# Optimization experiments

Hardware: AMD Instinct MI355X
Metric: run time of the kernel (lower is better)

Reference implementation:

```python
import jax, jax.numpy as jnp
import numpy as np

EPS = 1e-5  # GroupNorm eps


def setup_inputs() -> dict:
    key = jax.random.key(0)
    ks = jax.random.split(key, 12)
    D, H, I = 512, 8, 64
    B, L = 2, 1024
    g = 0.01  # xavier gain used in reset_parameters
    inp = {
        "x": jax.random.normal(ks[0], (B, L, D), jnp.float32),
        "w_z": jax.random.normal(ks[1], (D, D), jnp.float32) * g,
        "b_z": jnp.zeros((D,), jnp.float32),
        "w_za": jax.random.normal(ks[2], (D, D), jnp.float32) * g,
        "b_za": jnp.zeros((D,), jnp.float32),
        "w_ang": jax.random.normal(ks[3], (D, H), jnp.float32) * g,
        "b_ang": jnp.zeros((H,), jnp.float32),
        "w_abs": jax.random.normal(ks[4], (D, H), jnp.float32) * g,
        "b_abs": jnp.zeros((H,), jnp.float32),
        "w_y": jax.random.normal(ks[5], (D, D), jnp.float32) * g,
        "b_y": jnp.zeros((D,), jnp.float32),
        "w_ya": jax.random.normal(ks[6], (D, D), jnp.float32) * g,
        "b_ya": jnp.zeros((D,), jnp.float32),
        "gn_w": jnp.ones((H,), jnp.float32),
        "gn_b": jnp.zeros((H,), jnp.float32),
        "lc_r": jax.random.normal(ks[7], (H, I), jnp.float32),
        "lc_i": jax.random.normal(ks[8], (H, I), jnp.float32),
    }
    return inp


def reference(x, w_z, b_z, w_za, b_za, w_ang, b_ang, w_abs, b_abs,
              w_y, b_y, w_ya, b_ya, gn_w, gn_b, lc_r, lc_i):
    B, L, D = x.shape
    H = gn_w.shape[0]
    I = D // H
    silu = jax.nn.silu
    xf = x.astype(jnp.float32)

    # gated value, promoted to complex:  [B, L, H, I]
    z = ((xf @ w_z + b_z) * silu(xf @ w_za + b_za)).astype(jnp.complex64).reshape(B, L, H, I)

    # per-head log-decay phazor: [B, L, H] complex
    scale = (0.001 ** jnp.linspace(0.0, 1.0, H)).astype(jnp.float32)
    ln_ph = (silu(xf @ w_ang + b_ang) * 1j - jax.nn.sigmoid(xf @ w_abs + b_abs)) * scale

    # FFT of ones => circular conv with ones = cumulative sum along axis 1
    ones_fft = jnp.fft.fft(jnp.ones((L,), jnp.float32), n=2 * L)

    # ln_phazor repeated over m then tril(-1) over the LAST TWO dims (m, h),
    # exactly matching torch.Tensor.tril semantics on a 'b l m h' tensor.
    masked = jnp.tril(jnp.broadcast_to(ln_ph[:, :, None, :], (B, L, L, H)), -1)
    mfft = jnp.fft.fft(masked, n=2 * L, axis=1)
    mconv = jnp.fft.ifft(mfft * ones_fft[None, :, None, None], axis=1)[:, :L]
    ph_masked = jnp.tril(jnp.exp(mconv))  # tril over (m, h)

    h_inner = jnp.einsum('blmh,bmhi->blhi', ph_masked, z)

    pfft = jnp.fft.fft(ln_ph, n=2 * L, axis=1)
    pconv = jnp.fft.ifft(pfft * ones_fft[None, :, None], axis=1)[:, :L]
    last_conv = lc_r + 1j * lc_i  # [H, I] complex (last_conv_init broadcast over batch)
    h_cross = jnp.exp(pconv)[..., None] * last_conv[None, None]  # [B, L, H, I]

    h = (h_inner + h_cross).real  # [B, L, H, I]

    # GroupNorm(H groups, H channels) on (B*L, H, I): per-(sample, head) norm over I
    mean = h.mean(axis=-1, keepdims=True)
    var = h.var(axis=-1, keepdims=True)
    hn = (h - mean) / jnp.sqrt(var + EPS) * gn_w[:, None] + gn_b[:, None]
    h_norm = hn.reshape(B, L, D)

    y = (h_norm @ w_y + b_y) * silu(xf @ w_ya + b_ya)
    return y.astype(x.dtype)
```

## Files before the change

kernel.cpp:

```cpp
#include <hip/hip_runtime.h>
#include <math.h>

#define D_ 512
#define H_ 8
#define I_ 64
#define L_ 1024

typedef __attribute__((ext_vector_type(8))) short short8;
typedef __attribute__((ext_vector_type(4))) float f32x4;

__device__ __forceinline__ float sigmoidf_(float x) { return 1.f / (1.f + expf(-x)); }
__device__ __forceinline__ float siluf_(float x) { return x / (1.f + expf(-x)); }

__device__ __forceinline__ unsigned short f2bf(float f) {
    unsigned u = __float_as_uint(f);
    u += 0x7fffu + ((u >> 16) & 1u);
    return (unsigned short)(u >> 16);
}
__device__ __forceinline__ float bf2f(unsigned short v) {
    return __uint_as_float((unsigned)v << 16);
}

__global__ __launch_bounds__(256) void k1_prep(
    const float* __restrict__ x,
    const float* __restrict__ w0, const float* __restrict__ w1,
    const float* __restrict__ w2, const float* __restrict__ w3,
    unsigned short* __restrict__ t0, unsigned short* __restrict__ t1,
    unsigned short* __restrict__ t2, unsigned short* __restrict__ t3,
    const float* __restrict__ w_ang, const float* __restrict__ b_ang,
    const float* __restrict__ w_abs, const float* __restrict__ b_abs,
    float* __restrict__ a_out, float* __restrict__ r_out)
{
    __shared__ float sm[64][65];
    const int tid = threadIdx.x;
    const int bid = blockIdx.x;
    if (bid < 256) {
        int zsel = bid >> 6, tile = bid & 63;
        const float* src = zsel == 0 ? w0 : zsel == 1 ? w1 : zsel == 2 ? w2 : w3;
        unsigned short* dst = zsel == 0 ? t0 : zsel == 1 ? t1 : zsel == 2 ? t2 : t3;
        const int k0 = (tile >> 3) * 64, n0 = (tile & 7) * 64;
#pragma unroll
        for (int i = 0; i < 16; ++i) {
            int idx = tid + i * 256;
            int rr = idx >> 6, cc = idx & 63;
            sm[rr][cc] = src[(size_t)(k0 + rr) * 512 + n0 + cc];
        }
        __syncthreads();
#pragma unroll
        for (int i = 0; i < 16; ++i) {
            int idx = tid + i * 256;
            int rr = idx >> 6, cc = idx & 63;
            dst[(size_t)(n0 + rr) * 512 + k0 + cc] = f2bf(sm[cc][rr]);
        }
        return;
    }
    {
        int t = bid - 256;
        const int s = tid & 3, c = (tid >> 2) & 15, r = tid >> 6;
        const int n = t * 4 + r;
        const int h = c & 7;
        const float* wp = (c < 8) ? w_ang : w_abs;
        const float* xr = x + (size_t)n * D_;
        float acc = 0.f;
#pragma unroll 4
        for (int i = 0; i < 128; ++i) {
            int k = i * 4 + s;
            acc = fmaf(xr[k], wp[k * H_ + h], acc);
        }
        acc += __shfl_xor(acc, 1);
        acc += __shfl_xor(acc, 2);
        if (s == 0) {
            const float scale = expf(-6.9077552789821368f * (h * (1.0f / 7.0f)));
            if (c < 8) { float p = acc + b_ang[h]; a_out[(size_t)n * H_ + h] = siluf_(p) * scale; }
            else       { float p = acc + b_abs[h]; r_out[(size_t)n * H_ + h] = sigmoidf_(p) * scale; }
        }
    }
}

__global__ __launch_bounds__(256) void k2_gemm3_scan(
    const float* __restrict__ x,
    const unsigned short* __restrict__ Wz, const unsigned short* __restrict__ Wza,
    const unsigned short* __restrict__ Wya,
    const float* __restrict__ b_z, const float* __restrict__ b_za, const float* __restrict__ b_ya,
    unsigned short* __restrict__ gateb, float* __restrict__ Zs_part, float* __restrict__ zdiag,
    const float* __restrict__ a_arr, const float* __restrict__ r_arr,
    float* __restrict__ Si, float* __restrict__ Sr)
{
    __shared__ short As[2][2048];
    __shared__ short Bs[2][3][2048];
    __shared__ float red[64][8];
    __shared__ float2 buf[2][256];
    const int tid = threadIdx.x;

    if ((int)blockIdx.y < 2) {
        const int b = blockIdx.y, h = blockIdx.x;
        float2 v[4];
        float2 run = make_float2(0.f, 0.f);
        const size_t base = ((size_t)b * L_ + tid * 4) * H_ + h;
#pragma unroll
        for (int j = 0; j < 4; ++j) {
            run.x += a_arr[base + j * H_];
            run.y += r_arr[base + j * H_];
            v[j] = run;
        }
        buf[0][tid] = run;
        __syncthreads();
        int src = 0;
        for (int off = 1; off < 256; off <<= 1) {
            float2 val = buf[src][tid];
            if (tid >= off) { float2 p = buf[src][tid - off]; val.x += p.x; val.y += p.y; }
            buf[src ^ 1][tid] = val;
            src ^= 1;
            __syncthreads();
        }
        float2 excl = make_float2(0.f, 0.f);
        if (tid > 0) excl = buf[src][tid - 1];
#pragma unroll
        for (int j = 0; j < 4; ++j) {
            Si[base + j * H_] = v[j].x + excl.x;
            Sr[base + j * H_] = -(v[j].y + excl.y);
        }
        return;
    }

    const int lane = tid & 63, w = tid >> 6;
    const int wm = w >> 1, wn = w & 1;
    const int bx = blockIdx.x;
    const int rblk = (int)blockIdx.y - 2;
    const int row0 = rblk * 64, col0 = bx * 64;

    const f32x4 zf = {0.f, 0.f, 0.f, 0.f};
    f32x4 accz[2][2], accza[2][2], accya[2][2];
#pragma unroll
    for (int a = 0; a < 2; ++a)
#pragma unroll
        for (int bq = 0; bq < 2; ++bq) { accz[a][bq] = zf; accza[a][bq] = zf; accya[a][bq] = zf; }

    const int sr = tid >> 2, sc = tid & 3;
    const int sld = sr * 64 + ((sc ^ ((sr >> 1) & 3)) << 4);
    const float* gAx = x + (size_t)(row0 + sr) * 512 + sc * 8;
    const unsigned short* gWz  = Wz  + (size_t)(col0 + sr) * 512 + sc * 8;
    const unsigned short* gWza = Wza + (size_t)(col0 + sr) * 512 + sc * 8;
    const unsigned short* gWya = Wya + (size_t)(col0 + sr) * 512 + sc * 8;

    float4 ra0, ra1; int4 rz, rza, rya;
#define K2_LOAD(K) { ra0 = *(const float4*)(gAx + (K)); ra1 = *(const float4*)(gAx + (K) + 4); \
                     rz  = *(const int4*)(gWz  + (K)); rza = *(const int4*)(gWza + (K)); \
                     rya = *(const int4*)(gWya + (K)); }
#define K2_WRITE(BUF) { short8 ab; \
                        ab[0]=(short)f2bf(ra0.x); ab[1]=(short)f2bf(ra0.y); \
                        ab[2]=(short)f2bf(ra0.z); ab[3]=(short)f2bf(ra0.w); \
                        ab[4]=(short)f2bf(ra1.x); ab[5]=(short)f2bf(ra1.y); \
                        ab[6]=(short)f2bf(ra1.z); ab[7]=(short)f2bf(ra1.w); \
                        *(short8*)((char*)As[BUF] + sld) = ab; \
                        *(int4*)((char*)Bs[BUF][0] + sld) = rz; \
                        *(int4*)((char*)Bs[BUF][1] + sld) = rza; \
                        *(int4*)((char*)Bs[BUF][2] + sld) = rya; }

    K2_LOAD(0);
    K2_WRITE(0);
    K2_LOAD(32);
    __syncthreads();

    int cur = 0;
    for (int s = 0; s < 16; ++s) {
        if (s < 15) {
            K2_WRITE(cur ^ 1);
            if (s < 14) K2_LOAD((s + 2) * 32);
        }
        short8 af[2], bz[2], bza[2], bya[2];
#pragma unroll
        for (int fi = 0; fi < 2; ++fi) {
            int rr = wm * 32 + fi * 16 + (lane & 15);
            int off = rr * 64 + ((((lane >> 4)) ^ ((rr >> 1) & 3)) << 4);
            af[fi] = *(const short8*)((const char*)As[cur] + off);
        }
#pragma unroll
        for (int fj = 0; fj < 2; ++fj) {
            int rr = wn * 32 + fj * 16 + (lane & 15);
            int off = rr * 64 + ((((lane >> 4)) ^ ((rr >> 1) & 3)) << 4);
            bz[fj]  = *(const short8*)((const char*)Bs[cur][0] + off);
            bza[fj] = *(const short8*)((const char*)Bs[cur][1] + off);
            bya[fj] = *(const short8*)((const char*)Bs[cur][2] + off);
        }
#pragma unroll
        for (int fi = 0; fi < 2; ++fi)
#pragma unroll
            for (int fj = 0; fj < 2; ++fj) {
                accz[fi][fj]  = __builtin_amdgcn_mfma_f32_16x16x32_bf16(af[fi], bz[fj],  accz[fi][fj],  0, 0, 0);
                accza[fi][fj] = __builtin_amdgcn_mfma_f32_16x16x32_bf16(af[fi], bza[fj], accza[fi][fj], 0, 0, 0);
                accya[fi][fj] = __builtin_amdgcn_mfma_f32_16x16x32_bf16(af[fi], bya[fj], accya[fi][fj], 0, 0, 0);
            }
        __syncthreads();
        cur ^= 1;
    }

    const bool first = (rblk & 15) == 0;
    const int b8 = (rblk >> 4) * 8;
#pragma unroll
    for (int fj = 0; fj < 2; ++fj) {
        float lsum = 0.f;
        int lc = wn * 32 + fj * 16 + (lane & 15);
        int col = col0 + lc;
        float Bz = b_z[col], Bza = b_za[col], Bya = b_ya[col];
#pragma unroll
        for (int fi = 0; fi < 2; ++fi) {
#pragma unroll
            for (int q = 0; q < 4; ++q) {
                int lr = wm * 32 + fi * 16 + ((lane >> 4) << 2) + q;
                int row = row0 + lr;
                float pz = accz[fi][fj][q] + Bz;
                float pza = accza[fi][fj][q] + Bza;
                float v = pz * siluf_(pza);
                gateb[(size_t)row * 512 + col] = f2bf(siluf_(accya[fi][fj][q] + Bya));
                if (!first || lr > bx) lsum += v;
                if (first && lr == bx) zdiag[(b8 + bx) * 64 + lc] = v;
            }
        }
        red[lc][wm * 4 + (lane >> 4)] = lsum;
    }
    __syncthreads();
    if (tid < 64) {
        float s = 0.f;
#pragma unroll
        for (int j = 0; j < 8; ++j) s += red[tid][j];
        Zs_part[((size_t)rblk * 8 + bx) * 64 + tid] = s;
    }
}

__global__ __launch_bounds__(512) void k3_hgn_gemm_y(
    const unsigned short* __restrict__ Wy, const float* __restrict__ b_y,
    const unsigned short* __restrict__ gateb,
    const float* __restrict__ Sr, const float* __restrict__ Si,
    const float* __restrict__ Zs_part, const float* __restrict__ zdiag,
    const float* __restrict__ lc_r, const float* __restrict__ lc_i,
    const float* __restrict__ gn_w, const float* __restrict__ gn_b,
    float* __restrict__ y)
{
    __shared__ unsigned short hA[64][520];
    __shared__ short Bs[2][2048];
    __shared__ float Cr[8][65], Ci[8][65], Zd[8][65];
    const int tid = threadIdx.x;
    const int lane = tid & 63, w = tid >> 6;
    const int row0 = blockIdx.y * 64, col0 = blockIdx.x * 64;
    const int b = row0 >> 10;

    const int brow = tid >> 3, bsc = tid & 7;
    const size_t gB = (size_t)(col0 + brow) * 512 + bsc * 4;
    const int bwr = brow * 64 + (((bsc >> 1) ^ ((brow >> 1) & 3)) << 4) + (bsc & 1) * 8;
    int2 rw0 = *(const int2*)(Wy + gB);
    int2 rw1 = *(const int2*)(Wy + gB + 32);

    {
        int h = tid >> 6, i = tid & 63;
        float s = 0.f;
#pragma unroll
        for (int rb = 0; rb < 16; ++rb)
            s += Zs_part[(((size_t)b * 16 + rb) * 8 + h) * 64 + i];
        Cr[h][i] = s + lc_r[h * 64 + i];
        Ci[h][i] = lc_i[h * 64 + i];
        Zd[h][i] = zdiag[((size_t)b * 8 + h) * 64 + i];
    }
    __syncthreads();

    {
        const int r = tid >> 3, h = tid & 7;
        const int row = row0 + r;
        const float sr = Sr[(size_t)row * 8 + h];
        const float si = Si[(size_t)row * 8 + h];
        const float er = expf(sr);
        const float ca = er * cosf(si), sb = er * sinf(si);
        float sum = 0.f, sq = 0.f;
#pragma unroll 8
        for (int i = 0; i < 64; ++i) {
            float hv = Zd[h][i] + ca * Cr[h][i] - sb * Ci[h][i];
            sum += hv; sq += hv * hv;
        }
        const float mean = sum * (1.f / 64.f);
        const float inv = rsqrtf(sq * (1.f / 64.f) - mean * mean + 1e-5f);
        const float gw = gn_w[h] * inv;
        const float gb = gn_b[h] - mean * gw;
#pragma unroll
        for (int s8 = 0; s8 < 8; ++s8) {
            short8 pk;
#pragma unroll
            for (int j = 0; j < 8; ++j) {
                int i = s8 * 8 + j;
                float hv = Zd[h][i] + ca * Cr[h][i] - sb * Ci[h][i];
                pk[j] = (short)f2bf(hv * gw + gb);
            }
            int slot = (s8 + h) & 7;
            *(short8*)((char*)&hA[r][0] + h * 128 + slot * 16) = pk;
        }
    }
    *(int2*)((char*)Bs[0] + bwr) = rw0;
    __syncthreads();

    const int wm = w >> 2, wn = w & 3;
    const f32x4 zf = {0.f, 0.f, 0.f, 0.f};
    f32x4 acc[2] = {zf, zf};

    int cur = 0;
    for (int s = 0; s < 16; ++s) {
        if (s < 15) {
            *(int2*)((char*)Bs[cur ^ 1] + bwr) = rw1;
            if (s < 14) rw1 = *(const int2*)(Wy + gB + (s + 2) * 32);
        }
        const int k0 = s * 32;
        short8 af[2], bf;
        const int hk = k0 >> 6;
        const int t = ((k0 & 32) >> 3) + (lane >> 4);
        const int slot = (t + hk) & 7;
#pragma unroll
        for (int fi = 0; fi < 2; ++fi) {
            int rr = wm * 32 + fi * 16 + (lane & 15);
            af[fi] = *(const short8*)((const char*)&hA[rr][0] + hk * 128 + slot * 16);
        }
        {
            int rr = wn * 16 + (lane & 15);
            bf = *(const short8*)((const char*)Bs[cur] + rr * 64 + (((lane >> 4) ^ ((rr >> 1) & 3)) << 4));
        }
        acc[0] = __builtin_amdgcn_mfma_f32_16x16x32_bf16(af[0], bf, acc[0], 0, 0, 0);
        acc[1] = __builtin_amdgcn_mfma_f32_16x16x32_bf16(af[1], bf, acc[1], 0, 0, 0);
        __syncthreads();
        cur ^= 1;
    }

    const int col = col0 + wn * 16 + (lane & 15);
    const float By = b_y[col];
#pragma unroll
    for (int fi = 0; fi < 2; ++fi)
#pragma unroll
        for (int q = 0; q < 4; ++q) {
            int row = row0 + wm * 32 + fi * 16 + ((lane >> 4) << 2) + q;
            size_t idx = (size_t)row * 512 + col;
            y[idx] = (acc[fi][q] + By) * bf2f(gateb[idx]);
        }
}

extern "C" void kernel_launch(void* const* d_in, const int* in_sizes, int n_in,
                              void* d_out, int out_size, void* d_ws, size_t ws_size,
                              hipStream_t stream) {
    (void)n_in; (void)out_size; (void)ws_size;
    const float* x     = (const float*)d_in[0];
    const float* w_z   = (const float*)d_in[1];
    const float* b_z   = (const float*)d_in[2];
    const float* w_za  = (const float*)d_in[3];
    const float* b_za  = (const float*)d_in[4];
    const float* w_ang = (const float*)d_in[5];
    const float* b_ang = (const float*)d_in[6];
    const float* w_abs = (const float*)d_in[7];
    const float* b_abs = (const float*)d_in[8];
    const float* w_y   = (const float*)d_in[9];
    const float* b_y   = (const float*)d_in[10];
    const float* w_ya  = (const float*)d_in[11];
    const float* b_ya  = (const float*)d_in[12];
    const float* gn_w  = (const float*)d_in[13];
    const float* gn_b  = (const float*)d_in[14];
    const float* lc_r  = (const float*)d_in[15];
    const float* lc_i  = (const float*)d_in[16];
    float* y = (float*)d_out;

    const int BL = in_sizes[0] / D_;
    const int B  = BL / L_;

    unsigned short* wtz  = (unsigned short*)d_ws;
    unsigned short* wtza = wtz  + 512 * 512;
    unsigned short* wtya = wtza + 512 * 512;
    unsigned short* wty  = wtya + 512 * 512;
    unsigned short* gateb= wty  + 512 * 512;
    float* a_arr = (float*)(gateb + (size_t)BL * 512);
    float* r_arr = a_arr + (size_t)BL * H_;
    float* Si    = r_arr + (size_t)BL * H_;
    float* Sr    = Si    + (size_t)BL * H_;
    float* zdiag = Sr    + (size_t)BL * H_;
    float* Zs_part = zdiag + (size_t)B * H_ * I_;

    const int nby = BL / 64;

    k1_prep<<<256 + BL / 4, 256, 0, stream>>>(
        x, w_z, w_za, w_ya, w_y, wtz, wtza, wtya, wty,
        w_ang, b_ang, w_abs, b_abs, a_arr, r_arr);
    k2_gemm3_scan<<<dim3(8, nby + 2), 256, 0, stream>>>(
        x, wtz, wtza, wtya, b_z, b_za, b_ya,
        gateb, Zs_part, zdiag, a_arr, r_arr, Si, Sr);
    k3_hgn_gemm_y<<<dim3(8, nby), 512, 0, stream>>>(
        wty, b_y, gateb, Sr, Si, Zs_part, zdiag, lc_r, lc_i, gn_w, gn_b, y);
}
```

Before: 46.07 us.

## Use padded LDS rows and XCD-aware block mapping in GEMM kernels

Replaces the XOR-swizzled shared-memory tiles in both GEMM kernels with a padded row stride of 80 bytes, which simplifies the fragment address arithmetic. Flattens the k2 and k3 grids to 1D. In k2 the block index is remapped so that blocks landing on the same XCD under round-robin dispatch share row blocks of x, which is meant to improve L2 reuse. The padding raises LDS usage slightly, and the padded stride may bring back some bank conflicts compared with the swizzle.

After: 44.24 us. 4.0% less time.

```diff
diff --git a/kernel.cpp b/kernel.cpp
--- a/kernel.cpp
+++ b/kernel.cpp
@@ -20,6 +20,9 @@
 __device__ __forceinline__ float bf2f(unsigned short v) {
     return __uint_as_float((unsigned)v << 16);
 }
+
+#define RS 80
+#define RSS 40
 
 __global__ __launch_bounds__(256) void k1_prep(
     const float* __restrict__ x,
@@ -86,14 +89,15 @@
     const float* __restrict__ a_arr, const float* __restrict__ r_arr,
     float* __restrict__ Si, float* __restrict__ Sr)
 {
-    __shared__ short As[2][2048];
-    __shared__ short Bs[2][3][2048];
+    __shared__ short As[2][64 * RSS];
+    __shared__ short Bs[2][3][64 * RSS];
     __shared__ float red[64][8];
     __shared__ float2 buf[2][256];
     const int tid = threadIdx.x;
-
-    if ((int)blockIdx.y < 2) {
-        const int b = blockIdx.y, h = blockIdx.x;
+    const int bid = blockIdx.x;
+
+    if (bid < 16) {
+        const int b = bid >> 3, h = bid & 7;
         float2 v[4];
         float2 run = make_float2(0.f, 0.f);
         const size_t base = ((size_t)b * L_ + tid * 4) * H_ + h;
@@ -108,7 +112,7 @@
         int src = 0;
         for (int off = 1; off < 256; off <<= 1) {
             float2 val = buf[src][tid];
-            if (tid >= off) { float2 p = buf[src][tid - off]; val.x += p.x; val.y += p.y; }
+            if (tid >= off) { float2 q = buf[src][tid - off]; val.x += q.x; val.y += q.y; }
             buf[src ^ 1][tid] = val;
             src ^= 1;
             __syncthreads();
@@ -123,10 +127,11 @@
         return;
     }
 
+    const int u = bid - 16;
+    const int rblk = (u & 7) * 4 + (u >> 6);
+    const int bx = (u >> 3) & 7;
     const int lane = tid & 63, w = tid >> 6;
     const int wm = w >> 1, wn = w & 1;
-    const int bx = blockIdx.x;
-    const int rblk = (int)blockIdx.y - 2;
     const int row0 = rblk * 64, col0 = bx * 64;
 
     const f32x4 zf = {0.f, 0.f, 0.f, 0.f};
@@ -136,12 +141,12 @@
 #pragma unroll
         for (int bq = 0; bq < 2; ++bq) { accz[a][bq] = zf; accza[a][bq] = zf; accya[a][bq] = zf; }
 
-    const int sr = tid >> 2, sc = tid & 3;
-    const int sld = sr * 64 + ((sc ^ ((sr >> 1) & 3)) << 4);
-    const float* gAx = x + (size_t)(row0 + sr) * 512 + sc * 8;
-    const unsigned short* gWz  = Wz  + (size_t)(col0 + sr) * 512 + sc * 8;
-    const unsigned short* gWza = Wza + (size_t)(col0 + sr) * 512 + sc * 8;
-    const unsigned short* gWya = Wya + (size_t)(col0 + sr) * 512 + sc * 8;
+    const int sr_ = tid >> 2, sc_ = tid & 3;
+    const int sld = sr_ * RS + sc_ * 16;
+    const float* gAx = x + (size_t)(row0 + sr_) * 512 + sc_ * 8;
+    const unsigned short* gWz  = Wz  + (size_t)(col0 + sr_) * 512 + sc_ * 8;
+    const unsigned short* gWza = Wza + (size_t)(col0 + sr_) * 512 + sc_ * 8;
+    const unsigned short* gWya = Wya + (size_t)(col0 + sr_) * 512 + sc_ * 8;
 
     float4 ra0, ra1; int4 rz, rza, rya;
 #define K2_LOAD(K) { ra0 = *(const float4*)(gAx + (K)); ra1 = *(const float4*)(gAx + (K) + 4); \
@@ -169,19 +174,18 @@
             if (s < 14) K2_LOAD((s + 2) * 32);
         }
         short8 af[2], bz[2], bza[2], bya[2];
+        const int ck = (lane >> 4) << 4;
 #pragma unroll
         for (int fi = 0; fi < 2; ++fi) {
             int rr = wm * 32 + fi * 16 + (lane & 15);
-            int off = rr * 64 + ((((lane >> 4)) ^ ((rr >> 1) & 3)) << 4);
-            af[fi] = *(const short8*)((const char*)As[cur] + off);
+            af[fi] = *(const short8*)((const char*)As[cur] + rr * RS + ck);
         }
 #pragma unroll
         for (int fj = 0; fj < 2; ++fj) {
             int rr = wn * 32 + fj * 16 + (lane & 15);
-            int off = rr * 64 + ((((lane >> 4)) ^ ((rr >> 1) & 3)) << 4);
-            bz[fj]  = *(const short8*)((const char*)Bs[cur][0] + off);
-            bza[fj] = *(const short8*)((const char*)Bs[cur][1] + off);
-            bya[fj] = *(const short8*)((const char*)Bs[cur][2] + off);
+            bz[fj]  = *(const short8*)((const char*)Bs[cur][0] + rr * RS + ck);
+            bza[fj] = *(const short8*)((const char*)Bs[cur][1] + rr * RS + ck);
+            bya[fj] = *(const short8*)((const char*)Bs[cur][2] + rr * RS + ck);
         }
 #pragma unroll
         for (int fi = 0; fi < 2; ++fi)
@@ -194,6 +198,8 @@
         __syncthreads();
         cur ^= 1;
     }
+#undef K2_LOAD
+#undef K2_WRITE
 
     const bool first = (rblk & 15) == 0;
     const int b8 = (rblk >> 4) * 8;
@@ -238,16 +244,18 @@
     float* __restrict__ y)
 {
     __shared__ unsigned short hA[64][520];
-    __shared__ short Bs[2][2048];
+    __shared__ short Bs[2][64 * RSS];
     __shared__ float Cr[8][65], Ci[8][65], Zd[8][65];
     const int tid = threadIdx.x;
     const int lane = tid & 63, w = tid >> 6;
-    const int row0 = blockIdx.y * 64, col0 = blockIdx.x * 64;
+    const int cbx = blockIdx.x & 7;
+    const int rpair = blockIdx.x >> 3;
+    const int row0 = rpair * 64, col0 = cbx * 64;
     const int b = row0 >> 10;
 
     const int brow = tid >> 3, bsc = tid & 7;
     const size_t gB = (size_t)(col0 + brow) * 512 + bsc * 4;
-    const int bwr = brow * 64 + (((bsc >> 1) ^ ((brow >> 1) & 3)) << 4) + (bsc & 1) * 8;
+    const int bwr = brow * RS + bsc * 8;
     int2 rw0 = *(const int2*)(Wy + gB);
     int2 rw1 = *(const int2*)(Wy + gB + 32);
 
@@ -318,7 +326,7 @@
         }
         {
             int rr = wn * 16 + (lane & 15);
-            bf = *(const short8*)((const char*)Bs[cur] + rr * 64 + (((lane >> 4) ^ ((rr >> 1) & 3)) << 4));
+            bf = *(const short8*)((const char*)Bs[cur] + rr * RS + ((lane >> 4) << 4));
         }
         acc[0] = __builtin_amdgcn_mfma_f32_16x16x32_bf16(af[0], bf, acc[0], 0, 0, 0);
         acc[1] = __builtin_amdgcn_mfma_f32_16x16x32_bf16(af[1], bf, acc[1], 0, 0, 0);
@@ -376,14 +384,12 @@
     float* zdiag = Sr    + (size_t)BL * H_;
     float* Zs_part = zdiag + (size_t)B * H_ * I_;
 
-    const int nby = BL / 64;
-
     k1_prep<<<256 + BL / 4, 256, 0, stream>>>(
         x, w_z, w_za, w_ya, w_y, wtz, wtza, wtya, wty,
         w_ang, b_ang, w_abs, b_abs, a_arr, r_arr);
-    k2_gemm3_scan<<<dim3(8, nby + 2), 256, 0, stream>>>(
+    k2_gemm3_scan<<<16 + (BL / 64) * 8, 256, 0, stream>>>(
         x, wtz, wtza, wtya, b_z, b_za, b_ya,
         gateb, Zs_part, zdiag, a_arr, r_arr, Si, Sr);
-    k3_hgn_gemm_y<<<dim3(8, nby), 512, 0, stream>>>(
+    k3_hgn_gemm_y<<<(BL / 64) * 8, 512, 0, stream>>>(
         wty, b_y, gateb, Sr, Si, Zs_part, zdiag, lc_r, lc_i, gn_w, gn_b, y);
 }
```
